# Kernel tuning notes

Hardware: AMD Instinct MI355X
Metric: run time of the kernel (lower is better)

Reference implementation:

```python
import jax, jax.numpy as jnp
import numpy as np

B, S, E, H = 1, 4096, 768, 12
D = E // H  # head_dim = 64


def setup_inputs() -> dict:
    key = jax.random.key(0)
    ks = jax.random.split(key, 6)
    scale = 0.02
    x = jax.random.normal(ks[0], (B, S, E), dtype=jnp.float32)
    Wq = jax.random.normal(ks[1], (E, E), dtype=jnp.float32) * scale
    Wk = jax.random.normal(ks[2], (E, E), dtype=jnp.float32) * scale
    Wv = jax.random.normal(ks[3], (E, E), dtype=jnp.float32) * scale
    Wo = jax.random.normal(ks[4], (E, E), dtype=jnp.float32) * scale
    bo = jax.random.normal(ks[5], (E,), dtype=jnp.float32) * scale
    mask = jnp.tril(jnp.ones((S, S), dtype=bool))[None, None]  # [1,1,S,S] causal
    return {"x": x, "Wq": Wq, "Wk": Wk, "Wv": Wv, "Wo": Wo, "bo": bo, "mask": mask}


def reference(x, Wq, Wk, Wv, Wo, bo, mask):
    # projections (torch Linear: y = x @ W.T; here W stored as [E,E] applied as x@W)
    q = jnp.einsum('bse,ef->bsf', x, Wq).reshape(B, S, H, D).transpose(0, 2, 1, 3)
    k = jnp.einsum('bse,ef->bsf', x, Wk).reshape(B, S, H, D).transpose(0, 2, 1, 3)
    v = jnp.einsum('bse,ef->bsf', x, Wv).reshape(B, S, H, D).transpose(0, 2, 1, 3)
    scores = jnp.einsum('bhqd,bhkd->bhqk', q, k) / jnp.sqrt(jnp.float32(D))
    scores = jnp.where(mask, scores, -jnp.inf)
    attn = jax.nn.softmax(scores, axis=-1)  # dropout p=0 -> identity
    ctx = jnp.einsum('bhqk,bhkd->bhqd', attn, v)
    ctx = ctx.transpose(0, 2, 1, 3).reshape(B, S, E)
    return jnp.einsum('bse,ef->bsf', ctx, Wo) + bo
```

## Files before the change

### kernel.cpp

```cpp
#include <hip/hip_runtime.h>
#include <math.h>

#define S 4096
#define E 768
#define H 12
#define Dh 64
#define SCALE2 0.1803368801111204f

typedef short short8 __attribute__((ext_vector_type(8)));
typedef float floatx4 __attribute__((ext_vector_type(4)));

__device__ __forceinline__ unsigned short f2bf(float f) {
    union { float f; unsigned int i; } c; c.f = f;
    unsigned int i = c.i;
    return (unsigned short)((i + 0x7fffu + ((i >> 16) & 1u)) >> 16);
}

__device__ __forceinline__ unsigned int pk_bf16(float lo, float hi) {
#if __has_builtin(__builtin_amdgcn_cvt_pk_bf16_f32)
    typedef __bf16 bf16x2 __attribute__((ext_vector_type(2)));
    union { bf16x2 v; unsigned int u; } c;
    c.v = __builtin_amdgcn_cvt_pk_bf16_f32(lo, hi);
    return c.u;
#else
    union { float f; unsigned int i; } a, b; a.f = lo; b.f = hi;
    return ((a.i + 0x8000u) >> 16) | ((b.i + 0x8000u) & 0xFFFF0000u);
#endif
}

__device__ __forceinline__ unsigned int scale_pk(unsigned int u, float s) {
    union { unsigned int i; float f; } lo, hi;
    lo.i = u << 16; hi.i = u & 0xffff0000u;
    return pk_bf16(lo.f * s, hi.f * s);
}

__device__ __forceinline__ void pk_atomic_add_bf16(unsigned short* addr, unsigned int bits) {
    unsigned long long a = (unsigned long long)addr;
    asm volatile("global_atomic_pk_add_bf16 %0, %1, off" :: "v"(a), "v"(bits) : "memory");
}

__device__ __forceinline__ void gload_lds16(const unsigned short* g, unsigned short* l) {
    __builtin_amdgcn_global_load_lds(
        (const __attribute__((address_space(1))) unsigned int*)g,
        (__attribute__((address_space(3))) unsigned int*)l, 16, 0, 0);
}

__device__ __forceinline__ void pl32swap(unsigned &a, unsigned &b) {
#if __has_builtin(__builtin_amdgcn_permlane32_swap)
    typedef unsigned uint2v __attribute__((ext_vector_type(2)));
    uint2v r = __builtin_amdgcn_permlane32_swap(a, b, false, false);
    a = r[0]; b = r[1];
#else
    asm("s_nop 1\n\tv_permlane32_swap_b32 %0, %1\n\ts_nop 1" : "+v"(a), "+v"(b));
#endif
}
__device__ __forceinline__ void pl16swap(unsigned &a, unsigned &b) {
#if __has_builtin(__builtin_amdgcn_permlane16_swap)
    typedef unsigned uint2v __attribute__((ext_vector_type(2)));
    uint2v r = __builtin_amdgcn_permlane16_swap(a, b, false, false);
    a = r[0]; b = r[1];
#else
    asm("s_nop 1\n\tv_permlane16_swap_b32 %0, %1\n\ts_nop 1" : "+v"(a), "+v"(b));
#endif
}

__device__ __forceinline__ short8 quad_redist(unsigned a0, unsigned a1, unsigned a2, unsigned a3) {
    pl32swap(a0, a2); pl16swap(a0, a2);
    pl32swap(a1, a3); pl16swap(a1, a3);
    union { unsigned u[4]; short8 s; } r;
    r.u[0] = a0; r.u[1] = a1; r.u[2] = a2; r.u[3] = a3;
    return r.s;
}

__global__ __launch_bounds__(256)
void prep_kernel(const float* __restrict__ x, unsigned short* __restrict__ xb,
                 const float* __restrict__ s0, const float* __restrict__ s1,
                 const float* __restrict__ s2, const float* __restrict__ s3,
                 unsigned short* __restrict__ d0, unsigned short* __restrict__ d1,
                 unsigned short* __restrict__ d2, unsigned short* __restrict__ d3,
                 char* __restrict__ zbase) {
    __shared__ unsigned short tile[32][33];
    const int b = blockIdx.x;
    const int tid = threadIdx.x;
    if (b < 2304) {
        int z = b / 576, rem = b - z * 576;
        int bx = rem % 24, by = rem / 24;
        const float* src = (z == 0) ? s0 : (z == 1) ? s1 : (z == 2) ? s2 : s3;
        unsigned short* dst = (z == 0) ? d0 : (z == 1) ? d1 : (z == 2) ? d2 : d3;
        int tx = tid & 31, ty = tid >> 5;
        int xcol = bx * 32 + tx;
        int y0 = by * 32;
        for (int j = ty; j < 32; j += 8)
            tile[j][tx] = f2bf(src[(size_t)(y0 + j) * E + xcol]);
        __syncthreads();
        int x2 = y0 + tx;
        int y2 = bx * 32;
        for (int j = ty; j < 32; j += 8)
            dst[(size_t)(y2 + j) * E + x2] = tile[tx][j];
    } else if (b < 3840) {
        int i = ((b - 2304) * 256 + tid) * 8;
        float4 f0 = *reinterpret_cast<const float4*>(x + i);
        float4 f1 = *reinterpret_cast<const float4*>(x + i + 4);
        unsigned short u[8];
        u[0]=f2bf(f0.x); u[1]=f2bf(f0.y); u[2]=f2bf(f0.z); u[3]=f2bf(f0.w);
        u[4]=f2bf(f1.x); u[5]=f2bf(f1.y); u[6]=f2bf(f1.z); u[7]=f2bf(f1.w);
        *reinterpret_cast<uint4*>(xb + i) = *reinterpret_cast<uint4*>(u);
    } else {
        size_t i = (size_t)(b - 3840) * 16384 + (size_t)tid * 64;
        uint4 z4 = make_uint4(0u, 0u, 0u, 0u);
        *reinterpret_cast<uint4*>(zbase + i)      = z4;
        *reinterpret_cast<uint4*>(zbase + i + 16) = z4;
        *reinterpret_cast<uint4*>(zbase + i + 32) = z4;
        *reinterpret_cast<uint4*>(zbase + i + 48) = z4;
    }
}

__global__ __launch_bounds__(256)
void gemm_qkv(const unsigned short* __restrict__ A,
              const unsigned short* __restrict__ BT,
              unsigned short* __restrict__ Qb, unsigned short* __restrict__ Kb,
              unsigned short* __restrict__ VTb) {
    __shared__ unsigned short Asm[2][128 * 64];
    __shared__ unsigned short Bsm[2][128 * 64];
    const int tid  = threadIdx.x;
    const int wave = tid >> 6, lane = tid & 63;
    const int quad = lane >> 4, l16 = lane & 15;
    const int lrow = lane >> 3, lchunk = lane & 7;
    const int bb = blockIdx.x;
    const int xcd = bb & 7, j = bb >> 3;
    const int mt = (xcd >> 1) * 8 + (j & 7);
    const int nt = (xcd & 1) * 9 + (j >> 3);
    const int n0 = nt * 128;
    const int m0 = mt * 128;
    const int aw = wave >> 1, bw = wave & 1;

    floatx4 acc[4][4];
    #pragma unroll
    for (int at = 0; at < 4; at++)
        #pragma unroll
        for (int ct = 0; ct < 4; ct++)
            #pragma unroll
            for (int r = 0; r < 4; r++) acc[at][ct][r] = 0.f;

    auto stage = [&](int k0, int buf) {
        #pragma unroll
        for (int i = 0; i < 4; i++) {
            int rbase = wave * 32 + i * 8;
            int row   = rbase + lrow;
            int gc    = lchunk ^ (row & 7);
            gload_lds16(&A [(size_t)(m0 + row) * E + k0 + gc * 8], &Asm[buf][rbase * 64]);
            gload_lds16(&BT[(size_t)(n0 + row) * E + k0 + gc * 8], &Bsm[buf][rbase * 64]);
        }
    };

    stage(0, 0);
    stage(64, 1);

    for (int ki = 0; ki < 12; ki++) {
        const int cur = ki & 1;
        if (ki < 11) { asm volatile("s_waitcnt vmcnt(8)" ::: "memory"); }
        else         { asm volatile("s_waitcnt vmcnt(0)" ::: "memory"); }
        asm volatile("s_waitcnt lgkmcnt(0)" ::: "memory");
        __builtin_amdgcn_sched_barrier(0);
        __builtin_amdgcn_s_barrier();
        __builtin_amdgcn_sched_barrier(0);

        const unsigned short* As = Asm[cur];
        const unsigned short* Bs = Bsm[cur];
        #pragma unroll
        for (int kk = 0; kk < 2; kk++) {
            const int g = kk * 4 + quad;
            short8 af[4], bfr[4];
            #pragma unroll
            for (int t = 0; t < 4; t++) {
                int ar = aw * 64 + t * 16 + l16;
                af[t]  = *reinterpret_cast<const short8*>(&As[ar * 64 + (g ^ (ar & 7)) * 8]);
                int br = bw * 64 + t * 16 + l16;
                bfr[t] = *reinterpret_cast<const short8*>(&Bs[br * 64 + (g ^ (br & 7)) * 8]);
            }
            #pragma unroll
            for (int at = 0; at < 4; at++)
                #pragma unroll
                for (int ct = 0; ct < 4; ct++)
                    acc[at][ct] = __builtin_amdgcn_mfma_f32_16x16x32_bf16(af[at], bfr[ct], acc[at][ct], 0, 0, 0);
        }

        if (ki < 10) {
            __builtin_amdgcn_s_barrier();
            __builtin_amdgcn_sched_barrier(0);
            stage((ki + 2) * 64, cur);
        }
    }

    const int sec = n0 / 768;
    const int nb  = n0 - sec * 768 + bw * 64;
    if (sec == 2) {
        #pragma unroll
        for (int at = 0; at < 4; at++)
            #pragma unroll
            for (int ct = 0; ct < 4; ct++) {
                int nsec = nb + ct * 16 + l16, hh = nsec >> 6, d = nsec & 63;
                int s0i = m0 + aw * 64 + at * 16 + quad * 4;
                uint2 w2;
                w2.x = pk_bf16(acc[at][ct][0], acc[at][ct][1]);
                w2.y = pk_bf16(acc[at][ct][2], acc[at][ct][3]);
                *reinterpret_cast<uint2*>(&VTb[(size_t)hh * Dh * S + (size_t)d * S + s0i]) = w2;
            }
    } else {
        #pragma unroll
        for (int at = 0; at < 4; at++)
            #pragma unroll
            for (int ct = 0; ct < 4; ct++) {
                int nsec = nb + ct * 16 + l16, hh = nsec >> 6, d = nsec & 63;
                #pragma unroll
                for (int r = 0; r < 4; r++) {
                    int s = m0 + aw * 64 + at * 16 + quad * 4 + r;
                    float v = acc[at][ct][r];
                    if (sec == 0) Qb[(size_t)hh * S * Dh + (size_t)s * Dh + d] = f2bf(v * SCALE2);
                    else          Kb[(size_t)hh * S * Dh + (size_t)s * Dh + d] = f2bf(v);
                }
            }
    }
}

__global__ __launch_bounds__(256)
void gemm_out(const unsigned short* __restrict__ ctxp,
              const unsigned short* __restrict__ BT,
              const float* __restrict__ lsumf,
              float* __restrict__ outp, const float* __restrict__ bias) {
    __shared__ unsigned short Asm[2][128 * 64];
    __shared__ unsigned short Bsm[2][64 * 64];
    const int tid  = threadIdx.x;
    const int wave = tid >> 6, lane = tid & 63;
    const int quad = lane >> 4, l16 = lane & 15;
    const int lrow = lane >> 3, lchunk = lane & 7;
    const int bb = blockIdx.x;
    const int xcd = bb & 7, j = bb >> 3;
    const int mt = (xcd >> 1) * 8 + (j & 7);
    const int nt = (xcd & 1) * 6 + (j >> 3);
    const int n0 = nt * 64;
    const int m0 = mt * 128;
    const int arow = tid >> 1, ahalf = tid & 1;

    floatx4 acc[2][4];
    #pragma unroll
    for (int at = 0; at < 2; at++)
        #pragma unroll
        for (int ct = 0; ct < 4; ct++)
            #pragma unroll
            for (int r = 0; r < 4; r++) acc[at][ct][r] = 0.f;

    uint4 au[4]; float lf;
    auto loadA = [&](int k0) {
        const unsigned short* asrc = ctxp + (size_t)(m0 + arow) * E + k0 + ahalf * 32;
        au[0] = *reinterpret_cast<const uint4*>(asrc + 0);
        au[1] = *reinterpret_cast<const uint4*>(asrc + 8);
        au[2] = *reinterpret_cast<const uint4*>(asrc + 16);
        au[3] = *reinterpret_cast<const uint4*>(asrc + 24);
        lf = lsumf[(k0 >> 6) * S + m0 + arow];
    };
    auto writeA = [&](int buf) {
        float linv = 1.0f / lf;
        #pragma unroll
        for (int cc = 0; cc < 4; cc++) {
            uint4 w;
            w.x = scale_pk(au[cc].x, linv);
            w.y = scale_pk(au[cc].y, linv);
            w.z = scale_pk(au[cc].z, linv);
            w.w = scale_pk(au[cc].w, linv);
            int chunk = ahalf * 4 + cc;
            *reinterpret_cast<uint4*>(&Asm[buf][arow * 64 + (chunk ^ (arow & 7)) * 8]) = w;
        }
    };
    auto stageB = [&](int k0, int buf) {
        #pragma unroll
        for (int i = 0; i < 2; i++) {
            int rbase = wave * 16 + i * 8;
            int row   = rbase + lrow;
            int gc    = lchunk ^ (row & 7);
            gload_lds16(&BT[(size_t)(n0 + row) * E + k0 + gc * 8], &Bsm[buf][rbase * 64]);
        }
    };

    loadA(0);
    __builtin_amdgcn_sched_barrier(0);
    asm volatile("s_waitcnt vmcnt(0)" ::: "memory");
    writeA(0);
    __builtin_amdgcn_sched_barrier(0);
    stageB(0, 0);
    __builtin_amdgcn_sched_barrier(0);
    loadA(64);
    __builtin_amdgcn_sched_barrier(0);

    for (int ki = 0; ki < 12; ki++) {
        const int cur = ki & 1, nxt = cur ^ 1;
        if (ki <= 10) { asm volatile("s_waitcnt vmcnt(5)" ::: "memory"); }
        else          { asm volatile("s_waitcnt vmcnt(0)" ::: "memory"); }
        asm volatile("s_waitcnt lgkmcnt(0)" ::: "memory");
        __builtin_amdgcn_sched_barrier(0);
        __builtin_amdgcn_s_barrier();
        __builtin_amdgcn_sched_barrier(0);
        asm volatile("s_waitcnt vmcnt(0)" ::: "memory");
        if (ki < 11) writeA(nxt);
        __builtin_amdgcn_sched_barrier(0);
        if (ki < 11) stageB((ki + 1) * 64, nxt);
        if (ki <= 9) loadA((ki + 2) * 64);
        __builtin_amdgcn_sched_barrier(0);

        const unsigned short* As = Asm[cur];
        const unsigned short* Bs = Bsm[cur];
        #pragma unroll
        for (int kk = 0; kk < 2; kk++) {
            const int g = kk * 4 + quad;
            short8 af[2], bfr[4];
            #pragma unroll
            for (int t = 0; t < 2; t++) {
                int ar = wave * 32 + t * 16 + l16;
                af[t] = *reinterpret_cast<const short8*>(&As[ar * 64 + (g ^ (ar & 7)) * 8]);
            }
            #pragma unroll
            for (int ct = 0; ct < 4; ct++) {
                int br = ct * 16 + l16;
                bfr[ct] = *reinterpret_cast<const short8*>(&Bs[br * 64 + (g ^ (br & 7)) * 8]);
            }
            #pragma unroll
            for (int at = 0; at < 2; at++)
                #pragma unroll
                for (int ct = 0; ct < 4; ct++)
                    acc[at][ct] = __builtin_amdgcn_mfma_f32_16x16x32_bf16(af[at], bfr[ct], acc[at][ct], 0, 0, 0);
        }
    }

    #pragma unroll
    for (int at = 0; at < 2; at++)
        #pragma unroll
        for (int ct = 0; ct < 4; ct++) {
            int n = n0 + ct * 16 + l16;
            float bn = bias[n];
            #pragma unroll
            for (int r = 0; r < 4; r++) {
                int s = m0 + wave * 32 + at * 16 + quad * 4 + r;
                outp[(size_t)s * E + n] = acc[at][ct][r] + bn;
            }
        }
}

__global__ __launch_bounds__(512, 4)
void attn_kernel(const unsigned short* __restrict__ Q,
                 const unsigned short* __restrict__ K,
                 const unsigned short* __restrict__ VT,
                 unsigned short* __restrict__ ctxp,
                 float* __restrict__ lsumf) {
    __shared__ unsigned short Ksm[3][64 * 64];
    __shared__ unsigned short Vsm[3][64 * 64];
    const int tid  = threadIdx.x;
    const int wave = tid >> 6, lane = tid & 63;
    const int quad = lane >> 4, l16 = lane & 15;
    const int lrow = lane >> 3, lchunk = lane & 7;

    const int b = blockIdx.x;
    const int w = b / H;
    const int h = b - w * H;
    int Qb, ck, nck;
    if      (w < 16) { Qb = 15 - (w >> 3);              ck = w & 7;  nck = 8; }
    else if (w < 30) { int u = w - 16; Qb = 13 - u / 7;   ck = u % 7; nck = 7; }
    else if (w < 42) { int u = w - 30; Qb = 11 - u / 6;   ck = u % 6; nck = 6; }
    else if (w < 52) { int u = w - 42; Qb = 9  - u / 5;   ck = u % 5; nck = 5; }
    else if (w < 60) { int u = w - 52; Qb = 7 - (u >> 2); ck = u & 3; nck = 4; }
    else if (w < 66) { int u = w - 60; Qb = 5 - u / 3;    ck = u % 3; nck = 3; }
    else if (w < 70) { int u = w - 66; Qb = 3 - (u >> 1); ck = u & 1; nck = 2; }
    else             { Qb = 1 - (w - 70);                 ck = 0;     nck = 1; }
    const int ntiles = 4 * Qb + 4;
    const int kt0 = (ntiles * ck) / nck;
    const int kt1 = (ntiles * (ck + 1)) / nck;

    const int qs = Qb * 256 + wave * 32;

    const unsigned short* Qh = Q  + (size_t)h * S * Dh;
    const unsigned short* Kh = K  + (size_t)h * S * Dh;
    const unsigned short* Vh = VT + (size_t)h * Dh * S;

    short8 bq[2][2];
    #pragma unroll
    for (int st = 0; st < 2; st++)
        #pragma unroll
        for (int c = 0; c < 2; c++)
            bq[st][c] = *reinterpret_cast<const short8*>(
                &Qh[(size_t)(qs + st * 16 + l16) * Dh + c * 32 + quad * 8]);

    float lsum[2] = {0.f, 0.f};
    floatx4 o[2][4];
    #pragma unroll
    for (int st = 0; st < 2; st++)
        #pragma unroll
        for (int ct = 0; ct < 4; ct++)
            #pragma unroll
            for (int r = 0; r < 4; r++) o[st][ct][r] = 0.f;

    auto stage = [&](int kt, int buf) {
        int rbase = wave * 8;
        int row   = rbase + lrow;
        int gc    = lchunk ^ (row & 7);
        gload_lds16(&Kh[(size_t)(kt * 64 + row) * Dh + gc * 8], &Ksm[buf][rbase * 64]);
        gload_lds16(&Vh[(size_t)row * S + kt * 64 + gc * 8],    &Vsm[buf][rbase * 64]);
    };

    stage(kt0, 0);
    stage(kt0 + 1, 1);

    for (int kt = kt0; kt < kt1; kt++) {
        const int cur = (kt - kt0) % 3;
        if (kt + 1 < kt1) { asm volatile("s_waitcnt vmcnt(2)" ::: "memory"); }
        else              { asm volatile("s_waitcnt vmcnt(0)" ::: "memory"); }
        __builtin_amdgcn_sched_barrier(0);
        __builtin_amdgcn_s_barrier();
        __builtin_amdgcn_sched_barrier(0);
        if (kt + 2 < kt1) stage(kt + 2, (cur + 2) % 3);

        if (kt * 64 <= qs + 31) {
            floatx4 sc[2][4];
            #pragma unroll
            for (int st = 0; st < 2; st++)
                #pragma unroll
                for (int ct = 0; ct < 4; ct++)
                    #pragma unroll
                    for (int r = 0; r < 4; r++) sc[st][ct][r] = 0.f;
            __builtin_amdgcn_s_setprio(1);
            #pragma unroll
            for (int c = 0; c < 2; c++)
                #pragma unroll
                for (int ct = 0; ct < 4; ct++) {
                    int kr = ct * 16 + l16;
                    short8 ak = *reinterpret_cast<const short8*>(
                        &Ksm[cur][kr * 64 + ((c * 4 + quad) ^ (kr & 7)) * 8]);
                    sc[0][ct] = __builtin_amdgcn_mfma_f32_16x16x32_bf16(ak, bq[0][c], sc[0][ct], 0, 0, 0);
                    sc[1][ct] = __builtin_amdgcn_mfma_f32_16x16x32_bf16(ak, bq[1][c], sc[1][ct], 0, 0, 0);
                }
            __builtin_amdgcn_s_setprio(0);

            if (kt * 64 + 63 > qs) {
                #pragma unroll
                for (int st = 0; st < 2; st++) {
                    int qrow = qs + st * 16 + l16;
                    #pragma unroll
                    for (int ct = 0; ct < 4; ct++)
                        #pragma unroll
                        for (int r = 0; r < 4; r++) {
                            int kcol = kt * 64 + ct * 16 + quad * 4 + r;
                            if (kcol > qrow) sc[st][ct][r] = -INFINITY;
                        }
                }
            }

            unsigned Dp0[8], Dp1[8];
            #pragma unroll
            for (int ct = 0; ct < 4; ct++) {
                float a0 = __builtin_amdgcn_exp2f(sc[0][ct][0]);
                float a1 = __builtin_amdgcn_exp2f(sc[0][ct][1]);
                float a2 = __builtin_amdgcn_exp2f(sc[0][ct][2]);
                float a3 = __builtin_amdgcn_exp2f(sc[0][ct][3]);
                lsum[0] += a0 + a1 + a2 + a3;
                Dp0[ct * 2 + 0] = pk_bf16(a0, a1);
                Dp0[ct * 2 + 1] = pk_bf16(a2, a3);
                float b0 = __builtin_amdgcn_exp2f(sc[1][ct][0]);
                float b1 = __builtin_amdgcn_exp2f(sc[1][ct][1]);
                float b2 = __builtin_amdgcn_exp2f(sc[1][ct][2]);
                float b3 = __builtin_amdgcn_exp2f(sc[1][ct][3]);
                lsum[1] += b0 + b1 + b2 + b3;
                Dp1[ct * 2 + 0] = pk_bf16(b0, b1);
                Dp1[ct * 2 + 1] = pk_bf16(b2, b3);
            }

            __builtin_amdgcn_s_setprio(1);
            #pragma unroll
            for (int c = 0; c < 2; c++) {
                short8 ap0 = quad_redist(Dp0[4*c+0], Dp0[4*c+1], Dp0[4*c+2], Dp0[4*c+3]);
                short8 ap1 = quad_redist(Dp1[4*c+0], Dp1[4*c+1], Dp1[4*c+2], Dp1[4*c+3]);
                #pragma unroll
                for (int ct = 0; ct < 4; ct++) {
                    int vr = ct * 16 + l16;
                    short8 bv = *reinterpret_cast<const short8*>(
                        &Vsm[cur][vr * 64 + ((c * 4 + quad) ^ (vr & 7)) * 8]);
                    o[0][ct] = __builtin_amdgcn_mfma_f32_16x16x32_bf16(ap0, bv, o[0][ct], 0, 0, 0);
                    o[1][ct] = __builtin_amdgcn_mfma_f32_16x16x32_bf16(ap1, bv, o[1][ct], 0, 0, 0);
                }
            }
            __builtin_amdgcn_s_setprio(0);
        }
    }

    #pragma unroll
    for (int st = 0; st < 2; st++) {
        lsum[st] += __shfl_xor(lsum[st], 16, 64);
        lsum[st] += __shfl_xor(lsum[st], 32, 64);
    }
    if (quad == 0) {
        #pragma unroll
        for (int st = 0; st < 2; st++)
            atomicAdd(&lsumf[h * S + qs + st * 16 + l16], lsum[st]);
    }
    #pragma unroll
    for (int st = 0; st < 2; st++)
        #pragma unroll
        for (int r = 0; r < 4; r++) {
            int s = qs + st * 16 + quad * 4 + r;
            #pragma unroll
            for (int ct = 0; ct < 4; ct++) {
                float v  = o[st][ct][r];
                float vn = __shfl_xor(v, 1, 64);
                if ((l16 & 1) == 0)
                    pk_atomic_add_bf16(&ctxp[(size_t)s * E + h * Dh + ct * 16 + l16],
                                       pk_bf16(v, vn));
            }
        }
}

extern "C" void kernel_launch(void* const* d_in, const int* in_sizes, int n_in,
                              void* d_out, int out_size, void* d_ws, size_t ws_size,
                              hipStream_t stream) {
    const float* x  = (const float*)d_in[0];
    const float* Wq = (const float*)d_in[1];
    const float* Wk = (const float*)d_in[2];
    const float* Wv = (const float*)d_in[3];
    const float* Wo = (const float*)d_in[4];
    const float* bo = (const float*)d_in[5];
    float* out = (float*)d_out;

    char* ws = (char*)d_ws;
    const size_t WT = (size_t)E * E * 2;
    const size_t QB = (size_t)S * E * 2;
    unsigned short* WqT = (unsigned short*)(ws + 0 * WT);
    unsigned short* WkT = (unsigned short*)(ws + 1 * WT);
    unsigned short* WvT = (unsigned short*)(ws + 2 * WT);
    unsigned short* WoT = (unsigned short*)(ws + 3 * WT);
    unsigned short* xb  = (unsigned short*)(ws + 4 * WT + 0 * QB);
    unsigned short* Qbf = (unsigned short*)(ws + 4 * WT + 1 * QB);
    unsigned short* Kbf = (unsigned short*)(ws + 4 * WT + 2 * QB);
    unsigned short* VTb = (unsigned short*)(ws + 4 * WT + 3 * QB);
    unsigned short* ctxp  = (unsigned short*)(ws + 4 * WT + 4 * QB);
    float*          lsumf = (float*)(ws + 4 * WT + 5 * QB);

    prep_kernel<<<4236, 256, 0, stream>>>(
        x, xb, Wq, Wk, Wv, Wo, WqT, WkT, WvT, WoT, (char*)ctxp);

    gemm_qkv<<<576, 256, 0, stream>>>(xb, WqT, Qbf, Kbf, VTb);

    attn_kernel<<<864, 512, 0, stream>>>(Qbf, Kbf, VTb, ctxp, lsumf);

    gemm_out<<<384, 256, 0, stream>>>(ctxp, WoT, lsumf, out, bo);
}
```

Before: 230.3 us.

## Process 128-key tiles per barrier with split K/V staging buffers

The attention loop now stages 128-key tiles instead of 64, halving the number of barrier and wait iterations per block. K keeps a triple-buffered pipeline while V uses double buffering with a 16-chunk XOR swizzle over its 128-wide rows. Each tile is processed as two 64-column halves, with early exit past the causal diagonal. LDS use per block grows, which may lower occupancy, and the vmcnt accounting changes because each stage now issues two loads per buffer.

```diff
diff --git a/kernel.cpp b/kernel.cpp
--- a/kernel.cpp
+++ b/kernel.cpp
@@ -351,8 +351,8 @@
                  const unsigned short* __restrict__ VT,
                  unsigned short* __restrict__ ctxp,
                  float* __restrict__ lsumf) {
-    __shared__ unsigned short Ksm[3][64 * 64];
-    __shared__ unsigned short Vsm[3][64 * 64];
+    __shared__ unsigned short Ksm[3][128 * 64];
+    __shared__ unsigned short Vsm[2][64 * 128];
     const int tid  = threadIdx.x;
     const int wave = tid >> 6, lane = tid & 63;
     const int quad = lane >> 4, l16 = lane & 15;
@@ -370,7 +370,7 @@
     else if (w < 66) { int u = w - 60; Qb = 5 - u / 3;    ck = u % 3; nck = 3; }
     else if (w < 70) { int u = w - 66; Qb = 3 - (u >> 1); ck = u & 1; nck = 2; }
     else             { Qb = 1 - (w - 70);                 ck = 0;     nck = 1; }
-    const int ntiles = 4 * Qb + 4;
+    const int ntiles = 2 * Qb + 2;
     const int kt0 = (ntiles * ck) / nck;
     const int kt1 = (ntiles * (ck + 1)) / nck;
 
@@ -397,95 +397,117 @@
             #pragma unroll
             for (int r = 0; r < 4; r++) o[st][ct][r] = 0.f;
 
-    auto stage = [&](int kt, int buf) {
-        int rbase = wave * 8;
-        int row   = rbase + lrow;
-        int gc    = lchunk ^ (row & 7);
-        gload_lds16(&Kh[(size_t)(kt * 64 + row) * Dh + gc * 8], &Ksm[buf][rbase * 64]);
-        gload_lds16(&Vh[(size_t)row * S + kt * 64 + gc * 8],    &Vsm[buf][rbase * 64]);
+    auto stageK = [&](int kt, int buf) {
+        #pragma unroll
+        for (int i = 0; i < 2; i++) {
+            int rbase = wave * 16 + i * 8;
+            int row   = rbase + lrow;
+            int gc    = lchunk ^ (row & 7);
+            gload_lds16(&Kh[(size_t)(kt * 128 + row) * Dh + gc * 8], &Ksm[buf][rbase * 64]);
+        }
     };
-
-    stage(kt0, 0);
-    stage(kt0 + 1, 1);
+    auto stageV = [&](int kt, int buf) {
+        #pragma unroll
+        for (int i = 0; i < 2; i++) {
+            int rbase = wave * 8 + i * 4;
+            int row   = rbase + (lane >> 4);
+            int c     = (lane & 15) ^ (row & 15);
+            gload_lds16(&Vh[(size_t)row * S + kt * 128 + c * 8], &Vsm[buf][rbase * 128]);
+        }
+    };
+
+    stageV(kt0, 0);
+    stageK(kt0, 0);
+    if (kt0 + 1 < kt1) stageK(kt0 + 1, 1);
 
     for (int kt = kt0; kt < kt1; kt++) {
-        const int cur = (kt - kt0) % 3;
+        const int kc  = kt - kt0;
+        const int kb3 = kc % 3;
+        const int vb2 = kc & 1;
         if (kt + 1 < kt1) { asm volatile("s_waitcnt vmcnt(2)" ::: "memory"); }
         else              { asm volatile("s_waitcnt vmcnt(0)" ::: "memory"); }
         __builtin_amdgcn_sched_barrier(0);
         __builtin_amdgcn_s_barrier();
         __builtin_amdgcn_sched_barrier(0);
-        if (kt + 2 < kt1) stage(kt + 2, (cur + 2) % 3);
-
-        if (kt * 64 <= qs + 31) {
-            floatx4 sc[2][4];
-            #pragma unroll
-            for (int st = 0; st < 2; st++)
-                #pragma unroll
-                for (int ct = 0; ct < 4; ct++)
-                    #pragma unroll
-                    for (int r = 0; r < 4; r++) sc[st][ct][r] = 0.f;
-            __builtin_amdgcn_s_setprio(1);
-            #pragma unroll
-            for (int c = 0; c < 2; c++)
-                #pragma unroll
-                for (int ct = 0; ct < 4; ct++) {
-                    int kr = ct * 16 + l16;
-                    short8 ak = *reinterpret_cast<const short8*>(
-                        &Ksm[cur][kr * 64 + ((c * 4 + quad) ^ (kr & 7)) * 8]);
-                    sc[0][ct] = __builtin_amdgcn_mfma_f32_16x16x32_bf16(ak, bq[0][c], sc[0][ct], 0, 0, 0);
-                    sc[1][ct] = __builtin_amdgcn_mfma_f32_16x16x32_bf16(ak, bq[1][c], sc[1][ct], 0, 0, 0);
-                }
-            __builtin_amdgcn_s_setprio(0);
-
-            if (kt * 64 + 63 > qs) {
-                #pragma unroll
-                for (int st = 0; st < 2; st++) {
-                    int qrow = qs + st * 16 + l16;
+        if (kt + 1 < kt1) stageV(kt + 1, vb2 ^ 1);
+        if (kt + 2 < kt1) stageK(kt + 2, (kb3 + 2) % 3);
+        __builtin_amdgcn_sched_barrier(0);
+
+        if (kt * 128 <= qs + 31) {
+            #pragma unroll 1
+            for (int hf = 0; hf < 2; hf++) {
+                const int colbase = kt * 128 + hf * 64;
+                if (colbase > qs + 31) break;
+
+                floatx4 sc[2][4];
+                #pragma unroll
+                for (int st = 0; st < 2; st++)
                     #pragma unroll
                     for (int ct = 0; ct < 4; ct++)
                         #pragma unroll
-                        for (int r = 0; r < 4; r++) {
-                            int kcol = kt * 64 + ct * 16 + quad * 4 + r;
-                            if (kcol > qrow) sc[st][ct][r] = -INFINITY;
-                        }
+                        for (int r = 0; r < 4; r++) sc[st][ct][r] = 0.f;
+                __builtin_amdgcn_s_setprio(1);
+                #pragma unroll
+                for (int c = 0; c < 2; c++)
+                    #pragma unroll
+                    for (int ct = 0; ct < 4; ct++) {
+                        int kr = hf * 64 + ct * 16 + l16;
+                        short8 ak = *reinterpret_cast<const short8*>(
+                            &Ksm[kb3][kr * 64 + (((c * 4 + quad) ^ (kr & 7))) * 8]);
+                        sc[0][ct] = __builtin_amdgcn_mfma_f32_16x16x32_bf16(ak, bq[0][c], sc[0][ct], 0, 0, 0);
+                        sc[1][ct] = __builtin_amdgcn_mfma_f32_16x16x32_bf16(ak, bq[1][c], sc[1][ct], 0, 0, 0);
+                    }
+                __builtin_amdgcn_s_setprio(0);
+
+                if (colbase + 63 > qs) {
+                    #pragma unroll
+                    for (int st = 0; st < 2; st++) {
+                        int qrow = qs + st * 16 + l16;
+                        #pragma unroll
+                        for (int ct = 0; ct < 4; ct++)
+                            #pragma unroll
+                            for (int r = 0; r < 4; r++) {
+                                int kcol = colbase + ct * 16 + quad * 4 + r;
+                                if (kcol > qrow) sc[st][ct][r] = -INFINITY;
+                            }
+                    }
                 }
-            }
-
-            unsigned Dp0[8], Dp1[8];
-            #pragma unroll
-            for (int ct = 0; ct < 4; ct++) {
-                float a0 = __builtin_amdgcn_exp2f(sc[0][ct][0]);
-                float a1 = __builtin_amdgcn_exp2f(sc[0][ct][1]);
-                float a2 = __builtin_amdgcn_exp2f(sc[0][ct][2]);
-                float a3 = __builtin_amdgcn_exp2f(sc[0][ct][3]);
-                lsum[0] += a0 + a1 + a2 + a3;
-                Dp0[ct * 2 + 0] = pk_bf16(a0, a1);
-                Dp0[ct * 2 + 1] = pk_bf16(a2, a3);
-                float b0 = __builtin_amdgcn_exp2f(sc[1][ct][0]);
-                float b1 = __builtin_amdgcn_exp2f(sc[1][ct][1]);
-                float b2 = __builtin_amdgcn_exp2f(sc[1][ct][2]);
-                float b3 = __builtin_amdgcn_exp2f(sc[1][ct][3]);
-                lsum[1] += b0 + b1 + b2 + b3;
-                Dp1[ct * 2 + 0] = pk_bf16(b0, b1);
-                Dp1[ct * 2 + 1] = pk_bf16(b2, b3);
-            }
-
-            __builtin_amdgcn_s_setprio(1);
-            #pragma unroll
-            for (int c = 0; c < 2; c++) {
-                short8 ap0 = quad_redist(Dp0[4*c+0], Dp0[4*c+1], Dp0[4*c+2], Dp0[4*c+3]);
-                short8 ap1 = quad_redist(Dp1[4*c+0], Dp1[4*c+1], Dp1[4*c+2], Dp1[4*c+3]);
+
+                unsigned Dp0[8], Dp1[8];
                 #pragma unroll
                 for (int ct = 0; ct < 4; ct++) {
-                    int vr = ct * 16 + l16;
-                    short8 bv = *reinterpret_cast<const short8*>(
-                        &Vsm[cur][vr * 64 + ((c * 4 + quad) ^ (vr & 7)) * 8]);
-                    o[0][ct] = __builtin_amdgcn_mfma_f32_16x16x32_bf16(ap0, bv, o[0][ct], 0, 0, 0);
-                    o[1][ct] = __builtin_amdgcn_mfma_f32_16x16x32_bf16(ap1, bv, o[1][ct], 0, 0, 0);
+                    float a0 = __builtin_amdgcn_exp2f(sc[0][ct][0]);
+                    float a1 = __builtin_amdgcn_exp2f(sc[0][ct][1]);
+                    float a2 = __builtin_amdgcn_exp2f(sc[0][ct][2]);
+                    float a3 = __builtin_amdgcn_exp2f(sc[0][ct][3]);
+                    lsum[0] += a0 + a1 + a2 + a3;
+                    Dp0[ct * 2 + 0] = pk_bf16(a0, a1);
+                    Dp0[ct * 2 + 1] = pk_bf16(a2, a3);
+                    float b0 = __builtin_amdgcn_exp2f(sc[1][ct][0]);
+                    float b1 = __builtin_amdgcn_exp2f(sc[1][ct][1]);
+                    float b2 = __builtin_amdgcn_exp2f(sc[1][ct][2]);
+                    float b3 = __builtin_amdgcn_exp2f(sc[1][ct][3]);
+                    lsum[1] += b0 + b1 + b2 + b3;
+                    Dp1[ct * 2 + 0] = pk_bf16(b0, b1);
+                    Dp1[ct * 2 + 1] = pk_bf16(b2, b3);
                 }
-            }
-            __builtin_amdgcn_s_setprio(0);
+
+                __builtin_amdgcn_s_setprio(1);
+                #pragma unroll
+                for (int c = 0; c < 2; c++) {
+                    short8 ap0 = quad_redist(Dp0[4*c+0], Dp0[4*c+1], Dp0[4*c+2], Dp0[4*c+3]);
+                    short8 ap1 = quad_redist(Dp1[4*c+0], Dp1[4*c+1], Dp1[4*c+2], Dp1[4*c+3]);
+                    #pragma unroll
+                    for (int ct = 0; ct < 4; ct++) {
+                        int vr = ct * 16 + l16;
+                        short8 bv = *reinterpret_cast<const short8*>(
+                            &Vsm[vb2][vr * 128 + (((hf * 8 + c * 4 + quad) ^ (vr & 15))) * 8]);
+                        o[0][ct] = __builtin_amdgcn_mfma_f32_16x16x32_bf16(ap0, bv, o[0][ct], 0, 0, 0);
+                        o[1][ct] = __builtin_amdgcn_mfma_f32_16x16x32_bf16(ap1, bv, o[1][ct], 0, 0, 0);
+                    }
+                }
+                __builtin_amdgcn_s_setprio(0);
+            }
         }
     }
 
```

Measured after the change: 229.6 us. About the same (-0.3%).
